# Kernel tuning notes

Hardware: AMD Instinct MI355X
Metric: run time of the kernel (lower is better)

Reference implementation:

```python
import jax, jax.numpy as jnp
import numpy as np

B, N, DIN = 1, 1024, 512
NF, DCOND, H = 4, 128, 8
HD = DIN // H


def layernorm(x, g, b, eps=1e-5):
    mu = jnp.mean(x, axis=-1, keepdims=True)
    var = jnp.var(x, axis=-1, keepdims=True)
    return (x - mu) * jax.lax.rsqrt(var + eps) * g + b


def modlin2d(x, code, w_c, ln_g, ln_b, W, b):
    # code: [dcond, nf]; w_c: [din, dcond] -> code_mod: [nf, 1, din]
    code_mod = layernorm((w_c @ code).T, ln_g, ln_b)[:, None, :]
    return jnp.matmul(x * code_mod, W.T) + b


def setup_inputs() -> dict:
    key = jax.random.key(0)
    ks = jax.random.split(key, 8)
    s = lambda d: 1.0 / np.sqrt(d)
    return {
        "x": jax.random.normal(ks[0], (B, N, DIN), jnp.float32),
        "compatibility": jax.random.uniform(ks[1], (B, NF, N), jnp.float32),
        "code": jax.random.normal(ks[2], (DCOND, NF), jnp.float32),
        "w_c": jax.random.normal(ks[3], (DIN, DCOND), jnp.float32) * s(DCOND),
        "W_qkv": jax.random.normal(ks[4], (3 * DIN, DIN), jnp.float32) * s(DIN),
        "b_qkv": jnp.zeros((3 * DIN,), jnp.float32),
        "W_proj": jax.random.normal(ks[5], (DIN, DIN), jnp.float32) * s(DIN),
        "b_proj": jnp.zeros((DIN,), jnp.float32),
        "ln_qkv_g": jnp.ones((DIN,), jnp.float32),
        "ln_qkv_b": jnp.zeros((DIN,), jnp.float32),
        "ln_proj_g": jnp.ones((DIN,), jnp.float32),
        "ln_proj_b": jnp.zeros((DIN,), jnp.float32),
    }


def reference(x, compatibility, code, w_c, W_qkv, b_qkv, W_proj, b_proj,
              ln_qkv_g, ln_qkv_b, ln_proj_g, ln_proj_b):
    b, n, e = x.shape
    hd = e // H
    scale = hd ** -0.5
    # QKV: [B, nf, N, 3*din] -> split into [3, B, H, nf, N, hd]
    qkv = modlin2d(x[:, None, :, :], code, w_c, ln_qkv_g, ln_qkv_b, W_qkv, b_qkv)
    qkv = qkv.reshape(b, NF, n, 3, H, hd).transpose(3, 0, 4, 1, 2, 5)
    q, k, v = qkv[0], qkv[1], qkv[2]
    # first softmax over scaled scores
    attn = jax.nn.softmax(jnp.einsum('bhfnd,bhfmd->bhfnm', q, k) * scale, axis=-1)
    # compatibility outer product: [B, N, N] (sums over function axis)
    compat = jnp.einsum('bfn,bfm->bnm', compatibility, compatibility)
    W_hat = attn * compat[:, None, None, :, :]
    # second softmax
    Wm = jax.nn.softmax(W_hat, axis=-1)
    y_hat = jnp.einsum('bhfnm,bhfmd->bhfnd', Wm, v)
    y_hat = y_hat.transpose(0, 2, 3, 1, 4).reshape(b, NF, n, e)
    y = modlin2d(y_hat, code, w_c, ln_proj_g, ln_proj_b, W_proj, b_proj)
    return y
```

## Files before the change

kernel.cpp:

```cpp
#include <hip/hip_runtime.h>
#include <hip/hip_bf16.h>
#include <math.h>

#define NTOK 1024
#define DIN  512
#define NF   4
#define DCOND 128
#define H    8
#define HD   64
#define NQKV 1536

typedef __attribute__((ext_vector_type(8))) short bf16x8;
typedef __attribute__((ext_vector_type(4))) float f32x4;
typedef __attribute__((ext_vector_type(4))) unsigned short us4;

__device__ __forceinline__ unsigned short f2b(float f) {
  union { float f; unsigned int u; } v; v.f = f;
  unsigned int r = v.u + 0x7fffu + ((v.u >> 16) & 1u);
  return (unsigned short)(r >> 16);
}

__device__ __forceinline__ float b2f(unsigned short h) {
  union { unsigned int u; float f; } v; v.u = ((unsigned int)h) << 16;
  return v.f;
}

__device__ __forceinline__ void gl_lds16(const void* g, void* l) {
  __builtin_amdgcn_global_load_lds(
      (const __attribute__((address_space(1))) unsigned int*)g,
      (__attribute__((address_space(3))) unsigned int*)l, 16, 0, 0);
}

__global__ void prep_convert(const float* __restrict__ code, const float* __restrict__ w_c,
                             const float* __restrict__ lnqg, const float* __restrict__ lnqb,
                             const float* __restrict__ lnpg, const float* __restrict__ lnpb,
                             const float* __restrict__ W_qkv, const float* __restrict__ W_proj,
                             float* __restrict__ cmq, float* __restrict__ cmp_,
                             unsigned short* __restrict__ Wqh, unsigned short* __restrict__ Wph) {
  if (blockIdx.x == 0) {
    int i = threadIdx.x;
    float t[NF] = {0.f, 0.f, 0.f, 0.f};
    for (int k = 0; k < DCOND; ++k) {
      float w = w_c[i * DCOND + k];
      float4 cd = *reinterpret_cast<const float4*>(&code[k * NF]);
      t[0] += w * cd.x; t[1] += w * cd.y; t[2] += w * cd.z; t[3] += w * cd.w;
    }
    __shared__ float buf[512];
    for (int f = 0; f < NF; ++f) {
      buf[i] = t[f]; __syncthreads();
      for (int s = 256; s > 0; s >>= 1) { if (i < s) buf[i] += buf[i + s]; __syncthreads(); }
      float mu = buf[0] * (1.f / 512.f); __syncthreads();
      float d = t[f] - mu;
      buf[i] = d * d; __syncthreads();
      for (int s = 256; s > 0; s >>= 1) { if (i < s) buf[i] += buf[i + s]; __syncthreads(); }
      float rstd = rsqrtf(buf[0] * (1.f / 512.f) + 1e-5f);
      float nv = d * rstd;
      cmq[f * DIN + i]  = nv * lnqg[i] + lnqb[i];
      cmp_[f * DIN + i] = nv * lnpg[i] + lnpb[i];
      __syncthreads();
    }
  } else {
    int e0 = ((blockIdx.x - 1) * 512 + threadIdx.x) * 8;
    const float* src; unsigned short* dst; int e;
    if (e0 < 786432) { src = W_qkv; dst = Wqh; e = e0; }
    else { src = W_proj; dst = Wph; e = e0 - 786432; }
    float4 a = *reinterpret_cast<const float4*>(&src[e]);
    float4 b = *reinterpret_cast<const float4*>(&src[e + 4]);
    us4 p0 = { f2b(a.x), f2b(a.y), f2b(a.z), f2b(a.w) };
    us4 p1 = { f2b(b.x), f2b(b.y), f2b(b.z), f2b(b.w) };
    *reinterpret_cast<us4*>(&dst[e]) = p0;
    *reinterpret_cast<us4*>(&dst[e + 4]) = p1;
  }
}

template<int NCOL, bool OUT_BF16, bool WRITE_VT>
__global__ __launch_bounds__(256, 2)
void gemm_mod(const float* __restrict__ Asrc, int aMask,
              const float* __restrict__ cm,
              const unsigned short* __restrict__ Wh,
              const float* __restrict__ bias,
              unsigned short* __restrict__ outH,
              float* __restrict__ outF,
              unsigned short* __restrict__ vT) {
  __shared__ __align__(16) unsigned short sA[128 * 40];
  __shared__ __align__(16) unsigned short sB[128 * 32];
  const int tid = threadIdx.x;
  const int lane = tid & 63, w = tid >> 6;
  const int li = lane & 15, g = lane >> 4;
  const int wr = (w >> 1) * 64, wc = (w & 1) * 64;
  const int row0 = blockIdx.y * 128, col0 = blockIdx.x * 128;
  const int f = row0 >> 10;
  const int sr = tid >> 1, skh = (tid & 1) * 16;
  const float* aRow = Asrc + (size_t)((row0 + sr) & aMask) * DIN + skh;
  const float* cmRow = cm + f * DIN + skh;

  f32x4 acc[4][4];
#pragma unroll
  for (int m = 0; m < 4; ++m)
#pragma unroll
    for (int n = 0; n < 4; ++n) acc[m][n] = (f32x4){0.f, 0.f, 0.f, 0.f};

  for (int k0 = 0; k0 < DIN; k0 += 32) {
    float4 x0 = *reinterpret_cast<const float4*>(aRow + k0);
    float4 x1 = *reinterpret_cast<const float4*>(aRow + k0 + 4);
    float4 x2 = *reinterpret_cast<const float4*>(aRow + k0 + 8);
    float4 x3 = *reinterpret_cast<const float4*>(aRow + k0 + 12);
    float4 c0 = *reinterpret_cast<const float4*>(cmRow + k0);
    float4 c1 = *reinterpret_cast<const float4*>(cmRow + k0 + 4);
    float4 c2 = *reinterpret_cast<const float4*>(cmRow + k0 + 8);
    float4 c3 = *reinterpret_cast<const float4*>(cmRow + k0 + 12);
    bf16x8 p0, p1;
    p0[0] = (short)f2b(x0.x * c0.x); p0[1] = (short)f2b(x0.y * c0.y);
    p0[2] = (short)f2b(x0.z * c0.z); p0[3] = (short)f2b(x0.w * c0.w);
    p0[4] = (short)f2b(x1.x * c1.x); p0[5] = (short)f2b(x1.y * c1.y);
    p0[6] = (short)f2b(x1.z * c1.z); p0[7] = (short)f2b(x1.w * c1.w);
    p1[0] = (short)f2b(x2.x * c2.x); p1[1] = (short)f2b(x2.y * c2.y);
    p1[2] = (short)f2b(x2.z * c2.z); p1[3] = (short)f2b(x2.w * c2.w);
    p1[4] = (short)f2b(x3.x * c3.x); p1[5] = (short)f2b(x3.y * c3.y);
    p1[6] = (short)f2b(x3.z * c3.z); p1[7] = (short)f2b(x3.w * c3.w);
    *reinterpret_cast<bf16x8*>(&sA[sr * 40 + skh]) = p0;
    *reinterpret_cast<bf16x8*>(&sA[sr * 40 + skh + 8]) = p1;
#pragma unroll
    for (int j = 0; j < 2; ++j) {
      int slot = w * 128 + j * 64 + lane;
      int bcol = slot >> 2, sp = slot & 3;
      int s = sp ^ ((bcol >> 1) & 3);
      gl_lds16(Wh + (size_t)(col0 + bcol) * DIN + k0 + s * 8, &sB[(w * 128 + j * 64) * 8]);
    }
    __syncthreads();
    bf16x8 aF[4], bF[4];
#pragma unroll
    for (int m = 0; m < 4; ++m)
      aF[m] = *reinterpret_cast<const bf16x8*>(&sA[(wr + m * 16 + li) * 40 + g * 8]);
#pragma unroll
    for (int n = 0; n < 4; ++n) {
      int bcol = wc + n * 16 + li;
      int slot = bcol * 4 + (g ^ ((bcol >> 1) & 3));
      bF[n] = *reinterpret_cast<const bf16x8*>(&sB[slot * 8]);
    }
#pragma unroll
    for (int m = 0; m < 4; ++m)
#pragma unroll
      for (int n = 0; n < 4; ++n)
        acc[m][n] = __builtin_amdgcn_mfma_f32_16x16x32_bf16(aF[m], bF[n], acc[m][n], 0, 0, 0);
    __syncthreads();
  }
#pragma unroll
  for (int n = 0; n < 4; ++n) {
    int col = col0 + wc + n * 16 + li;
    float bb = bias[col];
#pragma unroll
    for (int m = 0; m < 4; ++m) {
      int rb = row0 + wr + m * 16 + g * 4;
      f32x4 v = acc[m][n];
      if constexpr (OUT_BF16) {
        if (WRITE_VT && col >= 1024) {
          int tok0 = rb & 1023;
          us4 pk;
#pragma unroll
          for (int r = 0; r < 4; ++r) pk[r] = f2b(v[r] + bb);
          *reinterpret_cast<us4*>(&vT[((size_t)(f * 512 + (col - 1024))) * NTOK + tok0]) = pk;
        } else {
#pragma unroll
          for (int r = 0; r < 4; ++r)
            outH[(size_t)(rb + r) * NCOL + col] = f2b(v[r] + bb);
        }
      } else {
#pragma unroll
        for (int r = 0; r < 4; ++r)
          outF[(size_t)(rb + r) * NCOL + col] = v[r] + bb;
      }
    }
  }
}

__global__ __launch_bounds__(256, 2)
void attn_mfma(const unsigned short* __restrict__ qkvh,
               const unsigned short* __restrict__ vTh,
               const float* __restrict__ comp,
               float* __restrict__ yhat) {
  __shared__ __align__(16) unsigned short sK[64 * 64];
  __shared__ __align__(16) unsigned short sVT[64 * 64];
  __shared__ __align__(16) unsigned short sW[4][16 * 72];
  __shared__ float scomp[4096];
  const int tid = threadIdx.x, lane = tid & 63, w = tid >> 6;
  const int li = lane & 15, g = lane >> 4;
  const int qt = blockIdx.x;
  const int h = blockIdx.y >> 2, f = blockIdx.y & 3;

  for (int i = tid * 4; i < 4096; i += 1024)
    *reinterpret_cast<float4*>(&scomp[i]) = *reinterpret_cast<const float4*>(&comp[i]);

  const int qrow0 = qt * 64 + w * 16;
  const unsigned short* qbase = qkvh + ((size_t)(f * NTOK + qrow0 + li)) * NQKV + h * HD;
  bf16x8 aq[2];
  aq[0] = *reinterpret_cast<const bf16x8*>(qbase + g * 8);
  aq[1] = *reinterpret_cast<const bf16x8*>(qbase + 32 + g * 8);

  float crow[4][4];
#pragma unroll
  for (int ff = 0; ff < 4; ++ff)
#pragma unroll
    for (int r = 0; r < 4; ++r)
      crow[ff][r] = comp[ff * NTOK + qrow0 + g * 4 + r];

  const unsigned short* kb = qkvh + ((size_t)(f * NTOK)) * NQKV + DIN + h * HD;
  const unsigned short* vb = vTh + ((size_t)(f * DIN + h * HD)) * NTOK;

  float mrow[4], lrow[4];
#pragma unroll
  for (int r = 0; r < 4; ++r) { mrow[r] = -1e30f; lrow[r] = 0.f; }

  for (int t = 0; t < 16; ++t) {
    __syncthreads();
#pragma unroll
    for (int j = 0; j < 2; ++j) {
      int slot = w * 128 + j * 64 + lane;
      int tok = slot >> 3, sp = slot & 7, s = sp ^ (tok & 7);
      gl_lds16(kb + (size_t)(t * 64 + tok) * NQKV + s * 8, &sK[(w * 128 + j * 64) * 8]);
    }
    __syncthreads();
    bf16x8 bk[4][2];
#pragma unroll
    for (int cf = 0; cf < 4; ++cf)
#pragma unroll
      for (int ks = 0; ks < 2; ++ks) {
        int tok = cf * 16 + li, s = ks * 4 + g;
        bk[cf][ks] = *reinterpret_cast<const bf16x8*>(&sK[(tok * 8 + (s ^ (tok & 7))) * 8]);
      }
    f32x4 accs[4];
#pragma unroll
    for (int cf = 0; cf < 4; ++cf) accs[cf] = (f32x4){0.f, 0.f, 0.f, 0.f};
#pragma unroll
    for (int ks = 0; ks < 2; ++ks)
#pragma unroll
      for (int cf = 0; cf < 4; ++cf)
        accs[cf] = __builtin_amdgcn_mfma_f32_16x16x32_bf16(aq[ks], bk[cf][ks], accs[cf], 0, 0, 0);
#pragma unroll
    for (int r = 0; r < 4; ++r) {
      float v0 = accs[0][r] * 0.125f, v1 = accs[1][r] * 0.125f;
      float v2 = accs[2][r] * 0.125f, v3 = accs[3][r] * 0.125f;
      float tm = fmaxf(fmaxf(v0, v1), fmaxf(v2, v3));
#pragma unroll
      for (int o = 8; o > 0; o >>= 1) tm = fmaxf(tm, __shfl_xor(tm, o));
      float nm = fmaxf(mrow[r], tm);
      float ssum = __expf(v0 - nm) + __expf(v1 - nm) + __expf(v2 - nm) + __expf(v3 - nm);
#pragma unroll
      for (int o = 8; o > 0; o >>= 1) ssum += __shfl_xor(ssum, o);
      lrow[r] = lrow[r] * __expf(mrow[r] - nm) + ssum;
      mrow[r] = nm;
    }
  }
  float inv_l[4];
#pragma unroll
  for (int r = 0; r < 4; ++r) inv_l[r] = 1.f / lrow[r];

  f32x4 acco[4];
  float sum2[4] = {0.f, 0.f, 0.f, 0.f};
#pragma unroll
  for (int cf = 0; cf < 4; ++cf) acco[cf] = (f32x4){0.f, 0.f, 0.f, 0.f};
  unsigned short* wbuf = &sW[w][0];

  for (int t = 0; t < 16; ++t) {
    __syncthreads();
#pragma unroll
    for (int j = 0; j < 2; ++j) {
      int slot = w * 128 + j * 64 + lane;
      int tok = slot >> 3, sp = slot & 7, s = sp ^ (tok & 7);
      gl_lds16(kb + (size_t)(t * 64 + tok) * NQKV + s * 8, &sK[(w * 128 + j * 64) * 8]);
    }
#pragma unroll
    for (int j = 0; j < 2; ++j) {
      int slot = w * 128 + j * 64 + lane;
      int d = slot >> 3, sp = slot & 7, s = sp ^ (d & 7);
      gl_lds16(vb + (size_t)d * NTOK + t * 64 + s * 8, &sVT[(w * 128 + j * 64) * 8]);
    }
    __syncthreads();
    bf16x8 bk[4][2];
#pragma unroll
    for (int cf = 0; cf < 4; ++cf)
#pragma unroll
      for (int ks = 0; ks < 2; ++ks) {
        int tok = cf * 16 + li, s = ks * 4 + g;
        bk[cf][ks] = *reinterpret_cast<const bf16x8*>(&sK[(tok * 8 + (s ^ (tok & 7))) * 8]);
      }
    f32x4 accs[4];
#pragma unroll
    for (int cf = 0; cf < 4; ++cf) accs[cf] = (f32x4){0.f, 0.f, 0.f, 0.f};
#pragma unroll
    for (int ks = 0; ks < 2; ++ks)
#pragma unroll
      for (int cf = 0; cf < 4; ++cf)
        accs[cf] = __builtin_amdgcn_mfma_f32_16x16x32_bf16(aq[ks], bk[cf][ks], accs[cf], 0, 0, 0);
#pragma unroll
    for (int cf = 0; cf < 4; ++cf) {
      int col = t * 64 + cf * 16 + li;
      float c0 = scomp[col], c1 = scomp[1024 + col];
      float c2 = scomp[2048 + col], c3 = scomp[3072 + col];
#pragma unroll
      for (int r = 0; r < 4; ++r) {
        float v = accs[cf][r] * 0.125f;
        float a = __expf(v - mrow[r]) * inv_l[r];
        float cc = crow[0][r] * c0 + crow[1][r] * c1 + crow[2][r] * c2 + crow[3][r] * c3;
        float tv = __expf(a * cc);
        unsigned short hv = f2b(tv);
        sum2[r] += b2f(hv);
        wbuf[(g * 4 + r) * 72 + cf * 16 + li] = hv;
      }
    }
    bf16x8 aw[2], bv[4][2];
#pragma unroll
    for (int ks = 0; ks < 2; ++ks)
      aw[ks] = *reinterpret_cast<const bf16x8*>(&wbuf[li * 72 + ks * 32 + g * 8]);
#pragma unroll
    for (int cf = 0; cf < 4; ++cf)
#pragma unroll
      for (int ks = 0; ks < 2; ++ks) {
        int d = cf * 16 + li, s = ks * 4 + g;
        bv[cf][ks] = *reinterpret_cast<const bf16x8*>(&sVT[(d * 8 + (s ^ (d & 7))) * 8]);
      }
#pragma unroll
    for (int ks = 0; ks < 2; ++ks)
#pragma unroll
      for (int cf = 0; cf < 4; ++cf)
        acco[cf] = __builtin_amdgcn_mfma_f32_16x16x32_bf16(aw[ks], bv[cf][ks], acco[cf], 0, 0, 0);
  }
#pragma unroll
  for (int r = 0; r < 4; ++r) {
#pragma unroll
    for (int o = 8; o > 0; o >>= 1) sum2[r] += __shfl_xor(sum2[r], o);
  }
#pragma unroll
  for (int cf = 0; cf < 4; ++cf)
#pragma unroll
    for (int r = 0; r < 4; ++r) {
      int qrow = qrow0 + g * 4 + r;
      yhat[((size_t)(f * NTOK + qrow)) * DIN + h * HD + cf * 16 + li] = acco[cf][r] / sum2[r];
    }
}

extern "C" void kernel_launch(void* const* d_in, const int* in_sizes, int n_in,
                              void* d_out, int out_size, void* d_ws, size_t ws_size,
                              hipStream_t stream) {
  const float* x      = (const float*)d_in[0];
  const float* compat = (const float*)d_in[1];
  const float* code   = (const float*)d_in[2];
  const float* w_c    = (const float*)d_in[3];
  const float* W_qkv  = (const float*)d_in[4];
  const float* b_qkv  = (const float*)d_in[5];
  const float* W_proj = (const float*)d_in[6];
  const float* b_proj = (const float*)d_in[7];
  const float* lnqg   = (const float*)d_in[8];
  const float* lnqb   = (const float*)d_in[9];
  const float* lnpg   = (const float*)d_in[10];
  const float* lnpb   = (const float*)d_in[11];
  float* out = (float*)d_out;

  float* cmq  = (float*)d_ws;
  float* cmp_ = cmq + NF * DIN;
  unsigned short* Wqh  = (unsigned short*)(cmp_ + NF * DIN);
  unsigned short* Wph  = Wqh + NQKV * DIN;
  unsigned short* qkvh = Wph + DIN * DIN;
  unsigned short* vTh  = qkvh + (size_t)NF * NTOK * NQKV;
  float* yhat = (float*)(vTh + (size_t)NF * DIN * NTOK);

  prep_convert<<<257, 512, 0, stream>>>(code, w_c, lnqg, lnqb, lnpg, lnpb,
                                        W_qkv, W_proj, cmq, cmp_, Wqh, Wph);
  gemm_mod<NQKV, true, true><<<dim3(12, 32), 256, 0, stream>>>(
      x, 1023, cmq, Wqh, b_qkv, qkvh, nullptr, vTh);
  attn_mfma<<<dim3(16, 32), 256, 0, stream>>>(qkvh, vTh, compat, yhat);
  gemm_mod<DIN, false, false><<<dim3(4, 32), 256, 0, stream>>>(
      yhat, 4095, cmp_, Wph, b_proj, nullptr, out, nullptr);
}
```

Measured before the change: 192.7 us.

## Pre-modulate activations to bf16 and double-buffer GEMM and attention LDS staging

Splits prep into a layernorm kernel (shuffle reductions, one-pass variance) and a conversion kernel that also writes the modulated x as bf16. Both GEMMs now read bf16 A through async global-to-LDS loads into double-buffered tiles, which removes the in-loop fp32 convert. The attention kernel double-buffers its K/V tiles, stores compatibility in LDS as bf16, and folds the projection modulation into a bf16 output. It also reorders the attention grid and raises occupancy hints. The cost is an extra kernel launch, extra LDS use, and small precision changes from bf16 compatibility values and one-pass variance.

New measurement: 174.0 us. 1.11x faster.

```diff
diff --git a/kernel.cpp b/kernel.cpp
--- a/kernel.cpp
+++ b/kernel.cpp
@@ -31,68 +31,94 @@
       (__attribute__((address_space(3))) unsigned int*)l, 16, 0, 0);
 }
 
-__global__ void prep_convert(const float* __restrict__ code, const float* __restrict__ w_c,
-                             const float* __restrict__ lnqg, const float* __restrict__ lnqb,
-                             const float* __restrict__ lnpg, const float* __restrict__ lnpb,
-                             const float* __restrict__ W_qkv, const float* __restrict__ W_proj,
-                             float* __restrict__ cmq, float* __restrict__ cmp_,
-                             unsigned short* __restrict__ Wqh, unsigned short* __restrict__ Wph) {
-  if (blockIdx.x == 0) {
-    int i = threadIdx.x;
-    float t[NF] = {0.f, 0.f, 0.f, 0.f};
-    for (int k = 0; k < DCOND; ++k) {
-      float w = w_c[i * DCOND + k];
-      float4 cd = *reinterpret_cast<const float4*>(&code[k * NF]);
-      t[0] += w * cd.x; t[1] += w * cd.y; t[2] += w * cd.z; t[3] += w * cd.w;
-    }
-    __shared__ float buf[512];
-    for (int f = 0; f < NF; ++f) {
-      buf[i] = t[f]; __syncthreads();
-      for (int s = 256; s > 0; s >>= 1) { if (i < s) buf[i] += buf[i + s]; __syncthreads(); }
-      float mu = buf[0] * (1.f / 512.f); __syncthreads();
-      float d = t[f] - mu;
-      buf[i] = d * d; __syncthreads();
-      for (int s = 256; s > 0; s >>= 1) { if (i < s) buf[i] += buf[i + s]; __syncthreads(); }
-      float rstd = rsqrtf(buf[0] * (1.f / 512.f) + 1e-5f);
-      float nv = d * rstd;
-      cmq[f * DIN + i]  = nv * lnqg[i] + lnqb[i];
-      cmp_[f * DIN + i] = nv * lnpg[i] + lnpb[i];
-      __syncthreads();
+__global__ void ln_kernel(const float* __restrict__ code, const float* __restrict__ w_c,
+                          const float* __restrict__ lnqg, const float* __restrict__ lnqb,
+                          const float* __restrict__ lnpg, const float* __restrict__ lnpb,
+                          float* __restrict__ cmq, float* __restrict__ cmp_) {
+  const int i = threadIdx.x;
+  const int w = i >> 6, lane = i & 63;
+  float t[NF] = {0.f, 0.f, 0.f, 0.f};
+  const float* wr = w_c + i * DCOND;
+#pragma unroll 8
+  for (int k = 0; k < DCOND; k += 4) {
+    float4 wv = *reinterpret_cast<const float4*>(wr + k);
+    float4 c0 = *reinterpret_cast<const float4*>(&code[k * 4]);
+    float4 c1 = *reinterpret_cast<const float4*>(&code[(k + 1) * 4]);
+    float4 c2 = *reinterpret_cast<const float4*>(&code[(k + 2) * 4]);
+    float4 c3 = *reinterpret_cast<const float4*>(&code[(k + 3) * 4]);
+    t[0] += wv.x * c0.x + wv.y * c1.x + wv.z * c2.x + wv.w * c3.x;
+    t[1] += wv.x * c0.y + wv.y * c1.y + wv.z * c2.y + wv.w * c3.y;
+    t[2] += wv.x * c0.z + wv.y * c1.z + wv.z * c2.z + wv.w * c3.z;
+    t[3] += wv.x * c0.w + wv.y * c1.w + wv.z * c2.w + wv.w * c3.w;
+  }
+  __shared__ float redS[8], redQ[8];
+#pragma unroll
+  for (int f = 0; f < NF; ++f) {
+    float s = t[f], q = t[f] * t[f];
+#pragma unroll
+    for (int o = 32; o > 0; o >>= 1) { s += __shfl_xor(s, o); q += __shfl_xor(q, o); }
+    if (lane == 0) { redS[w] = s; redQ[w] = q; }
+    __syncthreads();
+    float S = 0.f, Q = 0.f;
+#pragma unroll
+    for (int j = 0; j < 8; ++j) { S += redS[j]; Q += redQ[j]; }
+    float mu = S * (1.f / 512.f);
+    float var = Q * (1.f / 512.f) - mu * mu;
+    float rstd = rsqrtf(var + 1e-5f);
+    float nv = (t[f] - mu) * rstd;
+    cmq[f * DIN + i]  = nv * lnqg[i] + lnqb[i];
+    cmp_[f * DIN + i] = nv * lnpg[i] + lnpb[i];
+    __syncthreads();
+  }
+}
+
+__global__ void prep2_kernel(const float* __restrict__ W_qkv, const float* __restrict__ W_proj,
+                             const float* __restrict__ x, const float* __restrict__ cmq,
+                             unsigned short* __restrict__ Wqh, unsigned short* __restrict__ Wph,
+                             unsigned short* __restrict__ xm) {
+  const int bid = blockIdx.x, tid = threadIdx.x;
+  if (bid < 256) {
+    const float* src; unsigned short* dst; int e;
+    if (bid < 192) { src = W_qkv; dst = Wqh; e = bid * 4096 + tid * 16; }
+    else { src = W_proj; dst = Wph; e = (bid - 192) * 4096 + tid * 16; }
+#pragma unroll
+    for (int j = 0; j < 4; ++j) {
+      float4 a = *reinterpret_cast<const float4*>(&src[e + j * 4]);
+      us4 p = { f2b(a.x), f2b(a.y), f2b(a.z), f2b(a.w) };
+      *reinterpret_cast<us4*>(&dst[e + j * 4]) = p;
     }
   } else {
-    int e0 = ((blockIdx.x - 1) * 512 + threadIdx.x) * 8;
-    const float* src; unsigned short* dst; int e;
-    if (e0 < 786432) { src = W_qkv; dst = Wqh; e = e0; }
-    else { src = W_proj; dst = Wph; e = e0 - 786432; }
-    float4 a = *reinterpret_cast<const float4*>(&src[e]);
-    float4 b = *reinterpret_cast<const float4*>(&src[e + 4]);
-    us4 p0 = { f2b(a.x), f2b(a.y), f2b(a.z), f2b(a.w) };
-    us4 p1 = { f2b(b.x), f2b(b.y), f2b(b.z), f2b(b.w) };
-    *reinterpret_cast<us4*>(&dst[e]) = p0;
-    *reinterpret_cast<us4*>(&dst[e + 4]) = p1;
+    int e = (bid - 256) * 4096 + tid * 16;
+    int row = e >> 9, d = e & 511;
+    int f = row >> 10, n = row & 1023;
+    const float* xr = x + (size_t)n * DIN + d;
+    const float* cr = cmq + f * DIN + d;
+#pragma unroll
+    for (int j = 0; j < 4; ++j) {
+      float4 a = *reinterpret_cast<const float4*>(xr + j * 4);
+      float4 c = *reinterpret_cast<const float4*>(cr + j * 4);
+      us4 p = { f2b(a.x * c.x), f2b(a.y * c.y), f2b(a.z * c.z), f2b(a.w * c.w) };
+      *reinterpret_cast<us4*>(&xm[e + j * 4]) = p;
+    }
   }
 }
 
 template<int NCOL, bool OUT_BF16, bool WRITE_VT>
-__global__ __launch_bounds__(256, 2)
-void gemm_mod(const float* __restrict__ Asrc, int aMask,
-              const float* __restrict__ cm,
-              const unsigned short* __restrict__ Wh,
-              const float* __restrict__ bias,
-              unsigned short* __restrict__ outH,
-              float* __restrict__ outF,
-              unsigned short* __restrict__ vT) {
-  __shared__ __align__(16) unsigned short sA[128 * 40];
-  __shared__ __align__(16) unsigned short sB[128 * 32];
+__global__ __launch_bounds__(256, 3)
+void gemm_bb(const unsigned short* __restrict__ Ah,
+             const unsigned short* __restrict__ Wh,
+             const float* __restrict__ bias,
+             unsigned short* __restrict__ outH,
+             float* __restrict__ outF,
+             unsigned short* __restrict__ vT) {
+  __shared__ __align__(16) unsigned short sA[2][4096];
+  __shared__ __align__(16) unsigned short sB[2][4096];
   const int tid = threadIdx.x;
   const int lane = tid & 63, w = tid >> 6;
   const int li = lane & 15, g = lane >> 4;
   const int wr = (w >> 1) * 64, wc = (w & 1) * 64;
   const int row0 = blockIdx.y * 128, col0 = blockIdx.x * 128;
   const int f = row0 >> 10;
-  const int sr = tid >> 1, skh = (tid & 1) * 16;
-  const float* aRow = Asrc + (size_t)((row0 + sr) & aMask) * DIN + skh;
-  const float* cmRow = cm + f * DIN + skh;
 
   f32x4 acc[4][4];
 #pragma unroll
@@ -100,43 +126,36 @@
 #pragma unroll
     for (int n = 0; n < 4; ++n) acc[m][n] = (f32x4){0.f, 0.f, 0.f, 0.f};
 
-  for (int k0 = 0; k0 < DIN; k0 += 32) {
-    float4 x0 = *reinterpret_cast<const float4*>(aRow + k0);
-    float4 x1 = *reinterpret_cast<const float4*>(aRow + k0 + 4);
-    float4 x2 = *reinterpret_cast<const float4*>(aRow + k0 + 8);
-    float4 x3 = *reinterpret_cast<const float4*>(aRow + k0 + 12);
-    float4 c0 = *reinterpret_cast<const float4*>(cmRow + k0);
-    float4 c1 = *reinterpret_cast<const float4*>(cmRow + k0 + 4);
-    float4 c2 = *reinterpret_cast<const float4*>(cmRow + k0 + 8);
-    float4 c3 = *reinterpret_cast<const float4*>(cmRow + k0 + 12);
-    bf16x8 p0, p1;
-    p0[0] = (short)f2b(x0.x * c0.x); p0[1] = (short)f2b(x0.y * c0.y);
-    p0[2] = (short)f2b(x0.z * c0.z); p0[3] = (short)f2b(x0.w * c0.w);
-    p0[4] = (short)f2b(x1.x * c1.x); p0[5] = (short)f2b(x1.y * c1.y);
-    p0[6] = (short)f2b(x1.z * c1.z); p0[7] = (short)f2b(x1.w * c1.w);
-    p1[0] = (short)f2b(x2.x * c2.x); p1[1] = (short)f2b(x2.y * c2.y);
-    p1[2] = (short)f2b(x2.z * c2.z); p1[3] = (short)f2b(x2.w * c2.w);
-    p1[4] = (short)f2b(x3.x * c3.x); p1[5] = (short)f2b(x3.y * c3.y);
-    p1[6] = (short)f2b(x3.z * c3.z); p1[7] = (short)f2b(x3.w * c3.w);
-    *reinterpret_cast<bf16x8*>(&sA[sr * 40 + skh]) = p0;
-    *reinterpret_cast<bf16x8*>(&sA[sr * 40 + skh + 8]) = p1;
+  auto stage = [&](int buf, int k0) {
 #pragma unroll
     for (int j = 0; j < 2; ++j) {
       int slot = w * 128 + j * 64 + lane;
-      int bcol = slot >> 2, sp = slot & 3;
-      int s = sp ^ ((bcol >> 1) & 3);
-      gl_lds16(Wh + (size_t)(col0 + bcol) * DIN + k0 + s * 8, &sB[(w * 128 + j * 64) * 8]);
-    }
-    __syncthreads();
+      int r = slot >> 2, sp = slot & 3, s = sp ^ ((r >> 1) & 3);
+      gl_lds16(Ah + (size_t)(row0 + r) * DIN + k0 + s * 8, &sA[buf][(w * 128 + j * 64) * 8]);
+    }
+#pragma unroll
+    for (int j = 0; j < 2; ++j) {
+      int slot = w * 128 + j * 64 + lane;
+      int r = slot >> 2, sp = slot & 3, s = sp ^ ((r >> 1) & 3);
+      gl_lds16(Wh + (size_t)(col0 + r) * DIN + k0 + s * 8, &sB[buf][(w * 128 + j * 64) * 8]);
+    }
+  };
+
+  stage(0, 0);
+  __syncthreads();
+  for (int it = 0; it < 16; ++it) {
+    int buf = it & 1;
+    if (it < 15) stage(buf ^ 1, (it + 1) * 32);
     bf16x8 aF[4], bF[4];
 #pragma unroll
-    for (int m = 0; m < 4; ++m)
-      aF[m] = *reinterpret_cast<const bf16x8*>(&sA[(wr + m * 16 + li) * 40 + g * 8]);
+    for (int m = 0; m < 4; ++m) {
+      int ra = wr + m * 16 + li;
+      aF[m] = *reinterpret_cast<const bf16x8*>(&sA[buf][(ra * 4 + (g ^ ((ra >> 1) & 3))) * 8]);
+    }
 #pragma unroll
     for (int n = 0; n < 4; ++n) {
-      int bcol = wc + n * 16 + li;
-      int slot = bcol * 4 + (g ^ ((bcol >> 1) & 3));
-      bF[n] = *reinterpret_cast<const bf16x8*>(&sB[slot * 8]);
+      int cb = wc + n * 16 + li;
+      bF[n] = *reinterpret_cast<const bf16x8*>(&sB[buf][(cb * 4 + (g ^ ((cb >> 1) & 3))) * 8]);
     }
 #pragma unroll
     for (int m = 0; m < 4; ++m)
@@ -174,22 +193,31 @@
   }
 }
 
-__global__ __launch_bounds__(256, 2)
+__global__ __launch_bounds__(256, 3)
 void attn_mfma(const unsigned short* __restrict__ qkvh,
                const unsigned short* __restrict__ vTh,
                const float* __restrict__ comp,
-               float* __restrict__ yhat) {
-  __shared__ __align__(16) unsigned short sK[64 * 64];
-  __shared__ __align__(16) unsigned short sVT[64 * 64];
+               const float* __restrict__ cmp_,
+               unsigned short* __restrict__ ym) {
+  __shared__ __align__(16) unsigned short sK[2][4096];
+  __shared__ __align__(16) unsigned short sVT[2][4096];
   __shared__ __align__(16) unsigned short sW[4][16 * 72];
-  __shared__ float scomp[4096];
+  __shared__ __align__(16) unsigned short scompH[4096];
   const int tid = threadIdx.x, lane = tid & 63, w = tid >> 6;
   const int li = lane & 15, g = lane >> 4;
-  const int qt = blockIdx.x;
-  const int h = blockIdx.y >> 2, f = blockIdx.y & 3;
-
-  for (int i = tid * 4; i < 4096; i += 1024)
-    *reinterpret_cast<float4*>(&scomp[i]) = *reinterpret_cast<const float4*>(&comp[i]);
+  const int hf = blockIdx.x;
+  const int qt = blockIdx.y;
+  const int h = hf >> 2, f = hf & 3;
+
+  {
+    int e = tid * 16;
+#pragma unroll
+    for (int j = 0; j < 4; ++j) {
+      float4 a = *reinterpret_cast<const float4*>(&comp[e + j * 4]);
+      us4 p = { f2b(a.x), f2b(a.y), f2b(a.z), f2b(a.w) };
+      *reinterpret_cast<us4*>(&scompH[e + j * 4]) = p;
+    }
+  }
 
   const int qrow0 = qt * 64 + w * 16;
   const unsigned short* qbase = qkvh + ((size_t)(f * NTOK + qrow0 + li)) * NQKV + h * HD;
@@ -207,26 +235,39 @@
   const unsigned short* kb = qkvh + ((size_t)(f * NTOK)) * NQKV + DIN + h * HD;
   const unsigned short* vb = vTh + ((size_t)(f * DIN + h * HD)) * NTOK;
 
-  float mrow[4], lrow[4];
-#pragma unroll
-  for (int r = 0; r < 4; ++r) { mrow[r] = -1e30f; lrow[r] = 0.f; }
-
-  for (int t = 0; t < 16; ++t) {
-    __syncthreads();
+  auto stage_k = [&](int buf, int t) {
 #pragma unroll
     for (int j = 0; j < 2; ++j) {
       int slot = w * 128 + j * 64 + lane;
       int tok = slot >> 3, sp = slot & 7, s = sp ^ (tok & 7);
-      gl_lds16(kb + (size_t)(t * 64 + tok) * NQKV + s * 8, &sK[(w * 128 + j * 64) * 8]);
-    }
-    __syncthreads();
+      gl_lds16(kb + (size_t)(t * 64 + tok) * NQKV + s * 8, &sK[buf][(w * 128 + j * 64) * 8]);
+    }
+  };
+  auto stage_v = [&](int buf, int t) {
+#pragma unroll
+    for (int j = 0; j < 2; ++j) {
+      int slot = w * 128 + j * 64 + lane;
+      int d = slot >> 3, sp = slot & 7, s = sp ^ (d & 7);
+      gl_lds16(vb + (size_t)d * NTOK + t * 64 + s * 8, &sVT[buf][(w * 128 + j * 64) * 8]);
+    }
+  };
+
+  float mrow[4], lrow[4];
+#pragma unroll
+  for (int r = 0; r < 4; ++r) { mrow[r] = -1e30f; lrow[r] = 0.f; }
+
+  stage_k(0, 0);
+  __syncthreads();
+  for (int t = 0; t < 16; ++t) {
+    int buf = t & 1;
+    if (t < 15) stage_k(buf ^ 1, t + 1);
     bf16x8 bk[4][2];
 #pragma unroll
     for (int cf = 0; cf < 4; ++cf)
 #pragma unroll
       for (int ks = 0; ks < 2; ++ks) {
         int tok = cf * 16 + li, s = ks * 4 + g;
-        bk[cf][ks] = *reinterpret_cast<const bf16x8*>(&sK[(tok * 8 + (s ^ (tok & 7))) * 8]);
+        bk[cf][ks] = *reinterpret_cast<const bf16x8*>(&sK[buf][(tok * 8 + (s ^ (tok & 7))) * 8]);
       }
     f32x4 accs[4];
 #pragma unroll
@@ -250,6 +291,7 @@
       lrow[r] = lrow[r] * __expf(mrow[r] - nm) + ssum;
       mrow[r] = nm;
     }
+    __syncthreads();
   }
   float inv_l[4];
 #pragma unroll
@@ -261,28 +303,19 @@
   for (int cf = 0; cf < 4; ++cf) acco[cf] = (f32x4){0.f, 0.f, 0.f, 0.f};
   unsigned short* wbuf = &sW[w][0];
 
+  stage_k(0, 0);
+  stage_v(0, 0);
+  __syncthreads();
   for (int t = 0; t < 16; ++t) {
-    __syncthreads();
-#pragma unroll
-    for (int j = 0; j < 2; ++j) {
-      int slot = w * 128 + j * 64 + lane;
-      int tok = slot >> 3, sp = slot & 7, s = sp ^ (tok & 7);
-      gl_lds16(kb + (size_t)(t * 64 + tok) * NQKV + s * 8, &sK[(w * 128 + j * 64) * 8]);
-    }
-#pragma unroll
-    for (int j = 0; j < 2; ++j) {
-      int slot = w * 128 + j * 64 + lane;
-      int d = slot >> 3, sp = slot & 7, s = sp ^ (d & 7);
-      gl_lds16(vb + (size_t)d * NTOK + t * 64 + s * 8, &sVT[(w * 128 + j * 64) * 8]);
-    }
-    __syncthreads();
+    int buf = t & 1;
+    if (t < 15) { stage_k(buf ^ 1, t + 1); stage_v(buf ^ 1, t + 1); }
     bf16x8 bk[4][2];
 #pragma unroll
     for (int cf = 0; cf < 4; ++cf)
 #pragma unroll
       for (int ks = 0; ks < 2; ++ks) {
         int tok = cf * 16 + li, s = ks * 4 + g;
-        bk[cf][ks] = *reinterpret_cast<const bf16x8*>(&sK[(tok * 8 + (s ^ (tok & 7))) * 8]);
+        bk[cf][ks] = *reinterpret_cast<const bf16x8*>(&sK[buf][(tok * 8 + (s ^ (tok & 7))) * 8]);
       }
     f32x4 accs[4];
 #pragma unroll
@@ -295,8 +328,8 @@
 #pragma unroll
     for (int cf = 0; cf < 4; ++cf) {
       int col = t * 64 + cf * 16 + li;
-      float c0 = scomp[col], c1 = scomp[1024 + col];
-      float c2 = scomp[2048 + col], c3 = scomp[3072 + col];
+      float c0 = b2f(scompH[col]), c1 = b2f(scompH[1024 + col]);
+      float c2 = b2f(scompH[2048 + col]), c3 = b2f(scompH[3072 + col]);
 #pragma unroll
       for (int r = 0; r < 4; ++r) {
         float v = accs[cf][r] * 0.125f;
@@ -317,25 +350,30 @@
 #pragma unroll
       for (int ks = 0; ks < 2; ++ks) {
         int d = cf * 16 + li, s = ks * 4 + g;
-        bv[cf][ks] = *reinterpret_cast<const bf16x8*>(&sVT[(d * 8 + (s ^ (d & 7))) * 8]);
+        bv[cf][ks] = *reinterpret_cast<const bf16x8*>(&sVT[buf][(d * 8 + (s ^ (d & 7))) * 8]);
       }
 #pragma unroll
     for (int ks = 0; ks < 2; ++ks)
 #pragma unroll
       for (int cf = 0; cf < 4; ++cf)
         acco[cf] = __builtin_amdgcn_mfma_f32_16x16x32_bf16(aw[ks], bv[cf][ks], acco[cf], 0, 0, 0);
+    __syncthreads();
   }
 #pragma unroll
   for (int r = 0; r < 4; ++r) {
 #pragma unroll
     for (int o = 8; o > 0; o >>= 1) sum2[r] += __shfl_xor(sum2[r], o);
   }
+  float cscale[4];
+#pragma unroll
+  for (int cf = 0; cf < 4; ++cf) cscale[cf] = cmp_[f * DIN + h * HD + cf * 16 + li];
 #pragma unroll
   for (int cf = 0; cf < 4; ++cf)
 #pragma unroll
     for (int r = 0; r < 4; ++r) {
       int qrow = qrow0 + g * 4 + r;
-      yhat[((size_t)(f * NTOK + qrow)) * DIN + h * HD + cf * 16 + li] = acco[cf][r] / sum2[r];
+      ym[((size_t)(f * NTOK + qrow)) * DIN + h * HD + cf * 16 + li] =
+          f2b(acco[cf][r] / sum2[r] * cscale[cf]);
     }
 }
 
@@ -359,16 +397,17 @@
   float* cmq  = (float*)d_ws;
   float* cmp_ = cmq + NF * DIN;
   unsigned short* Wqh  = (unsigned short*)(cmp_ + NF * DIN);
-  unsigned short* Wph  = Wqh + NQKV * DIN;
-  unsigned short* qkvh = Wph + DIN * DIN;
+  unsigned short* Wph  = Wqh + (size_t)NQKV * DIN;
+  unsigned short* xm   = Wph + (size_t)DIN * DIN;
+  unsigned short* qkvh = xm + (size_t)NF * NTOK * DIN;
   unsigned short* vTh  = qkvh + (size_t)NF * NTOK * NQKV;
-  float* yhat = (float*)(vTh + (size_t)NF * DIN * NTOK);
-
-  prep_convert<<<257, 512, 0, stream>>>(code, w_c, lnqg, lnqb, lnpg, lnpb,
-                                        W_qkv, W_proj, cmq, cmp_, Wqh, Wph);
-  gemm_mod<NQKV, true, true><<<dim3(12, 32), 256, 0, stream>>>(
-      x, 1023, cmq, Wqh, b_qkv, qkvh, nullptr, vTh);
-  attn_mfma<<<dim3(16, 32), 256, 0, stream>>>(qkvh, vTh, compat, yhat);
-  gemm_mod<DIN, false, false><<<dim3(4, 32), 256, 0, stream>>>(
-      yhat, 4095, cmp_, Wph, b_proj, nullptr, out, nullptr);
-}
+  unsigned short* ym   = vTh + (size_t)NF * DIN * NTOK;
+
+  ln_kernel<<<1, 512, 0, stream>>>(code, w_c, lnqg, lnqb, lnpg, lnpb, cmq, cmp_);
+  prep2_kernel<<<768, 256, 0, stream>>>(W_qkv, W_proj, x, cmq, Wqh, Wph, xm);
+  gemm_bb<NQKV, true, true><<<dim3(12, 32), 256, 0, stream>>>(
+      xm, Wqh, b_qkv, qkvh, nullptr, vTh);
+  attn_mfma<<<dim3(32, 16), 256, 0, stream>>>(qkvh, vTh, compat, cmp_, ym);
+  gemm_bb<DIN, false, false><<<dim3(4, 32), 256, 0, stream>>>(
+      ym, Wph, b_proj, nullptr, out, nullptr);
+}
```
